# Kernel tuning notes

Hardware: AMD Instinct MI355X
Metric: run time of the kernel (lower is better)

The kernel has to match this reference:

```python
import jax, jax.numpy as jnp
import numpy as np
import math

B, S, D = 2, 4096, 512
H = 8
DH = D // H  # 64


def setup_inputs() -> dict:
    key = jax.random.key(0)
    k1, k2, k3, k4, k5 = jax.random.split(key, 5)
    scale = 1.0 / math.sqrt(D)
    return {
        "x": jax.random.normal(k1, (B, S, D), dtype=jnp.float32),
        "W_in": jax.random.normal(k2, (D, 3 * D), dtype=jnp.float32) * scale,
        "b_in": jax.random.normal(k3, (3 * D,), dtype=jnp.float32) * 0.01,
        "W_out": jax.random.normal(k4, (D, D), dtype=jnp.float32) * scale,
        "b_out": jax.random.normal(k5, (D,), dtype=jnp.float32) * 0.01,
        "causal_mask": 1,
    }


def reference(x, W_in, b_in, W_out, b_out, causal_mask):
    b, s, d = x.shape
    # fused QKV projection: (b, s, 3d)
    qkv = x @ W_in + b_in
    q, k, v = jnp.split(qkv, 3, axis=-1)
    # (b, s, d) -> (b, h, s, dh)
    def to_heads(t):
        return t.reshape(b, s, H, DH).transpose(0, 2, 1, 3)
    q, k, v = to_heads(q), to_heads(k), to_heads(v)
    # raw scores (b, h, s, s)
    scores = jnp.einsum("bhqd,bhkd->bhqk", q, k)
    if causal_mask:  # static python flag
        # upper-triangular (strictly above diag) -> -inf, applied pre-scaling
        # (matches source; -inf invariant under /sqrt(d_head))
        tri = jnp.triu(jnp.ones((s, s), dtype=bool), k=1)
        scores = jnp.where(tri, -jnp.inf, scores)
    attn = jax.nn.softmax(scores / math.sqrt(DH), axis=-1)
    out = jnp.einsum("bhqk,bhkd->bhqd", attn, v)
    out = out.transpose(0, 2, 1, 3).reshape(b, s, d)
    return out @ W_out + b_out
```

## Files before the change

### kernel.cpp

```cpp
#include <hip/hip_runtime.h>
#include <cstdint>
#include <cmath>

typedef unsigned short BF16;
typedef __attribute__((ext_vector_type(8))) short short8;
typedef __attribute__((ext_vector_type(4))) float f32x4;
typedef __attribute__((ext_vector_type(16))) float f32x16;
typedef __attribute__((ext_vector_type(2))) unsigned int uint2v;
typedef __attribute__((ext_vector_type(4))) unsigned int uint4v;

#define S_LEN 4096
#define DMODEL 512
#define NHEAD 8
#define DHEAD 64
#define BS 2
#define NROWS (BS * NHEAD * S_LEN)

__device__ __forceinline__ BF16 f2bf(float f) {
  union { float f; uint32_t u; } v; v.f = f;
  uint32_t r = (v.u + 0x7FFFu + ((v.u >> 16) & 1u)) >> 16;
  return (BF16)r;
}

__device__ __forceinline__ float bf2f(short u) {
  return __uint_as_float(((unsigned)(unsigned short)u) << 16);
}

__device__ __forceinline__ unsigned cvtpk(float a, float b) {
  unsigned r;
  asm volatile("v_cvt_pk_bf16_f32 %0, %1, %2" : "=v"(r) : "v"(a), "v"(b));
  return r;
}

__device__ __forceinline__ float partner32(float x, int hi) {
  unsigned a = __float_as_uint(x), b = a;
  uint2v r = __builtin_amdgcn_permlane32_swap(a, b, false, false);
  return __uint_as_float(hi ? r[0] : r[1]);
}

__device__ __forceinline__ void pl32(unsigned &a, unsigned &b) {
  uint2v r = __builtin_amdgcn_permlane32_swap(a, b, false, false);
  a = r[0]; b = r[1];
}

__device__ __forceinline__ void gload16(const void* g, void* lds) {
  __builtin_amdgcn_global_load_lds(
      (const __attribute__((address_space(1))) void*)g,
      (__attribute__((address_space(3))) void*)lds, 16, 0, 0);
}

#define MAX3(a, b, c) fmaxf(fmaxf((a), (b)), (c))
#define CS_CONST 0.18033688011112042f

__global__ __launch_bounds__(256) void cvt_x_k(const float* __restrict__ x,
                                               BF16* __restrict__ xb) {
  int i = blockIdx.x * 256 + threadIdx.x;
  float4 v = reinterpret_cast<const float4*>(x)[i];
  ushort4 o;
  o.x = f2bf(v.x); o.y = f2bf(v.y); o.z = f2bf(v.z); o.w = f2bf(v.w);
  reinterpret_cast<ushort4*>(xb)[i] = o;
}

__global__ __launch_bounds__(256) void trw_k(const float* __restrict__ W_in,
                                             const float* __restrict__ W_out,
                                             BF16* __restrict__ wint,
                                             BF16* __restrict__ woutt) {
  __shared__ float t[32][33];
  const bool second = blockIdx.x >= 48;
  const float* W = second ? W_out : W_in;
  BF16* Wt = second ? woutt : wint;
  const int N = second ? DMODEL : 3 * DMODEL;
  const int K = DMODEL;
  int n0 = (second ? ((int)blockIdx.x - 48) : (int)blockIdx.x) * 32;
  int k0 = blockIdx.y * 32;
  int tx = threadIdx.x & 31, ty = threadIdx.x >> 5;
#pragma unroll
  for (int i = 0; i < 4; ++i)
    t[ty + 8 * i][tx] = W[(size_t)(k0 + ty + 8 * i) * N + n0 + tx];
  __syncthreads();
#pragma unroll
  for (int i = 0; i < 4; ++i)
    Wt[(size_t)(n0 + ty + 8 * i) * K + k0 + tx] = f2bf(t[tx][ty + 8 * i]);
}

template <int MODE>
__global__ __launch_bounds__(256)
void gemm_k(const BF16* __restrict__ A, const BF16* __restrict__ Bt,
            const float* __restrict__ bias,
            BF16* __restrict__ Qb, BF16* __restrict__ Kb, BF16* __restrict__ Vc,
            float* __restrict__ Out) {
  __shared__ BF16 As[128 * 64];
  __shared__ BF16 Bs[128 * 64];
  const int tid = threadIdx.x;
  const int l = tid & 63, w = tid >> 6;
  const int wm = w >> 1, wn = w & 1;
  const int bm = blockIdx.x, bn = blockIdx.y;
  f32x4 acc[4][4] = {};

  for (int kt = 0; kt < 512 / 64; ++kt) {
#pragma unroll
    for (int i = 0; i < 4; ++i) {
      int ldsoff = i * 4096 + w * 1024;
      int off = ldsoff + l * 16;
      int row = off >> 7;
      int slot = ((off >> 4) & 7) ^ (row & 7);
      gload16(A + (size_t)(bm * 128 + row) * 512 + kt * 64 + slot * 8,
              (char*)As + ldsoff);
      gload16(Bt + (size_t)(bn * 128 + row) * 512 + kt * 64 + slot * 8,
              (char*)Bs + ldsoff);
    }
    __syncthreads();
    const char* Ab = (const char*)As;
    const char* Bb = (const char*)Bs;
    short8 af[4][2], bfr[4][2];
#pragma unroll
    for (int mf = 0; mf < 4; ++mf)
#pragma unroll
      for (int kk = 0; kk < 2; ++kk) {
        int row = wm * 64 + mf * 16 + (l & 15);
        int slot = ((l >> 4) + 4 * kk) ^ (row & 7);
        af[mf][kk] = *(const short8*)(Ab + row * 128 + slot * 16);
      }
#pragma unroll
    for (int nf = 0; nf < 4; ++nf)
#pragma unroll
      for (int kk = 0; kk < 2; ++kk) {
        int row = wn * 64 + nf * 16 + (l & 15);
        int slot = ((l >> 4) + 4 * kk) ^ (row & 7);
        bfr[nf][kk] = *(const short8*)(Bb + row * 128 + slot * 16);
      }
    __builtin_amdgcn_s_setprio(1);
#pragma unroll
    for (int kk = 0; kk < 2; ++kk)
#pragma unroll
      for (int mf = 0; mf < 4; ++mf)
#pragma unroll
        for (int nf = 0; nf < 4; ++nf)
          acc[mf][nf] = __builtin_amdgcn_mfma_f32_16x16x32_bf16(
              af[mf][kk], bfr[nf][kk], acc[mf][nf], 0, 0, 0);
    __builtin_amdgcn_s_setprio(0);
    __syncthreads();
  }

#pragma unroll
  for (int mf = 0; mf < 4; ++mf)
#pragma unroll
    for (int nf = 0; nf < 4; ++nf)
#pragma unroll
      for (int r = 0; r < 4; ++r) {
        int row = bm * 128 + wm * 64 + mf * 16 + ((l >> 4) << 2) + r;
        int col = bn * 128 + wn * 64 + nf * 16 + (l & 15);
        float v = acc[mf][nf][r] + bias[col];
        if (MODE == 0) {
          int sec = col >> 9, nl = col & 511;
          int h = nl >> 6, dh = nl & 63;
          int b = row >> 12, s = row & 4095;
          BF16* dst = sec == 0 ? Qb : (sec == 1 ? Kb : Vc);
          dst[(((size_t)(b * NHEAD + h)) * S_LEN + s) * DHEAD + dh] = f2bf(v);
        } else {
          Out[(size_t)row * DMODEL + col] = v;
        }
      }
}

__global__ __launch_bounds__(256)
void v_tr_k(const BF16* __restrict__ Vc, BF16* __restrict__ Vt) {
  __shared__ BF16 t[64][66];
  const int bh = blockIdx.y, st = blockIdx.x;
  const int tid = threadIdx.x;
  const int g = tid >> 3, c8 = (tid & 7) * 8;
#pragma unroll
  for (int p = 0; p < 2; ++p) {
    int s = p * 32 + g;
    short8 v = *(const short8*)(Vc + ((size_t)bh * S_LEN + st * 64 + s) * DHEAD + c8);
#pragma unroll
    for (int j = 0; j < 8; ++j) t[s][c8 + j] = (BF16)(unsigned short)v[j];
  }
  __syncthreads();
#pragma unroll
  for (int p = 0; p < 2; ++p) {
    int dh = p * 32 + g;
    short8 o;
#pragma unroll
    for (int j = 0; j < 8; ++j) o[j] = (short)t[c8 + j][dh];
    *(short8*)(Vt + ((size_t)bh * DHEAD + dh) * S_LEN + st * 64 + c8) = o;
  }
}

__global__ __launch_bounds__(256, 4)
void attn_k(const BF16* __restrict__ Qg, const BF16* __restrict__ Kg,
            const BF16* __restrict__ Vg, BF16* __restrict__ Opb,
            float* __restrict__ Ml) {
  __shared__ BF16 Kl[2][64 * 64];
  __shared__ BF16 Vl[2][64 * 64];
  const int tid = threadIdx.x, l = tid & 63, w = tid >> 6;
  const int hi = l >> 5, ln = l & 31;
  const int wgid = blockIdx.x;
  const int xcd = wgid & 7, j = wgid >> 3;
  const int bh = xcd * 2 + (j & 1);
  const int qr = (j >> 1) & 3;
  const int p = j >> 3;
  const BF16* Qh = Qg + (size_t)bh * S_LEN * DHEAD;
  const BF16* Kh = Kg + (size_t)bh * S_LEN * DHEAD;
  const BF16* Vh = Vg + (size_t)bh * DHEAD * S_LEN;
  const float CS = CS_CONST;
  short8 ones;
#pragma unroll
  for (int i = 0; i < 8; ++i) ones[i] = (short)0x3F80;

  int cur = 0;
  for (int rep = 0; rep < 2; ++rep) {
    const int qt = rep ? (31 - p) : p;
    const int qq = rep ? (3 - qr) : qr;
    const int NTf = 2 * qt + 2;
    const int kbase = (qq * NTf) >> 2;
    const int kend = ((qq + 1) * NTf) >> 2;
    const int NT = kend - kbase;
    const int q0w = qt * 128 + w * 32;
    const int qrow = q0w + ln;
    __syncthreads();

    short8 qb[4];
    {
      const BF16* qp = Qh + (size_t)qrow * DHEAD + hi * 8;
#pragma unroll
      for (int ks = 0; ks < 4; ++ks) qb[ks] = *(const short8*)(qp + ks * 16);
    }
    f32x16 oacc0 = {}, oacc1 = {}, lacc = {};
    float m_ = -INFINITY;

    auto stage = [&](int buf, int ktile) {
      const int kv0 = ktile * 64;
#pragma unroll
      for (int i = 0; i < 2; ++i) {
        int base = i * 4096 + w * 1024;
        int off = base + l * 16;
        int row = off >> 7;
        int slot = ((off >> 4) & 7) ^ (row & 7);
        gload16(Kh + (size_t)(kv0 + row) * DHEAD + slot * 8, (char*)Kl[buf] + base);
        gload16(Vh + (size_t)row * S_LEN + kv0 + slot * 8, (char*)Vl[buf] + base);
      }
    };

    if (NT > 0) {
      stage(cur, kbase);
      for (int kt = 0; kt < NT; ++kt) {
        __syncthreads();
        if (kt + 1 < NT) stage(cur ^ 1, kbase + kt + 1);
        const int kv0 = (kbase + kt) * 64;
        if (kv0 <= q0w + 31) {
          const char* Kb_ = (const char*)Kl[cur];
          f32x16 s0 = {}, s1 = {};
          __builtin_amdgcn_s_setprio(1);
#pragma unroll
          for (int ks = 0; ks < 4; ++ks) {
            int slot0 = (2 * ks + hi) ^ (ln & 7);
            short8 kf0 = *(const short8*)(Kb_ + ln * 128 + slot0 * 16);
            int row1 = 32 + ln;
            int slot1 = (2 * ks + hi) ^ (row1 & 7);
            short8 kf1 = *(const short8*)(Kb_ + row1 * 128 + slot1 * 16);
            s0 = __builtin_amdgcn_mfma_f32_32x32x16_bf16(kf0, qb[ks], s0, 0, 0, 0);
            s1 = __builtin_amdgcn_mfma_f32_32x32x16_bf16(kf1, qb[ks], s1, 0, 0, 0);
          }
          __builtin_amdgcn_s_setprio(0);
          if (kv0 + 63 > q0w) {
#pragma unroll
            for (int r = 0; r < 16; ++r) {
              int crow = (r & 3) + 8 * (r >> 2) + 4 * hi;
              if (kv0 + crow > qrow) s0[r] = -INFINITY;
              if (kv0 + 32 + crow > qrow) s1[r] = -INFINITY;
            }
          }
          float a0 = MAX3(s0[0], s0[1], s0[2]);
          float a1 = MAX3(s0[3], s0[4], s0[5]);
          float a2 = MAX3(s0[6], s0[7], s0[8]);
          float a3 = MAX3(s0[9], s0[10], s0[11]);
          float a4 = MAX3(s0[12], s0[13], s0[14]);
          float a5 = MAX3(s0[15], s1[0], s1[1]);
          float a6 = MAX3(s1[2], s1[3], s1[4]);
          float a7 = MAX3(s1[5], s1[6], s1[7]);
          float a8 = MAX3(s1[8], s1[9], s1[10]);
          float a9 = MAX3(s1[11], s1[12], s1[13]);
          float a10 = fmaxf(s1[14], s1[15]);
          float b0 = MAX3(a0, a1, a2);
          float b1 = MAX3(a3, a4, a5);
          float b2 = MAX3(a6, a7, a8);
          float b3 = fmaxf(a9, a10);
          float pmax = fmaxf(fmaxf(b0, b1), fmaxf(b2, b3));
          pmax = fmaxf(pmax, partner32(pmax, hi));
          bool need = (pmax - m_) * CS > 8.0f;
          if (__any(need)) {
            float mn = fmaxf(m_, pmax);
            float alpha = exp2f((m_ - mn) * CS);
            m_ = mn;
            lacc[0] *= alpha;
#pragma unroll
            for (int r = 0; r < 16; ++r) { oacc0[r] *= alpha; oacc1[r] *= alpha; }
          }
          const float mb = m_ * CS;
          float p0[16], p1[16];
#pragma unroll
          for (int r = 0; r < 16; ++r) p0[r] = exp2f(fmaf(s0[r], CS, -mb));
#pragma unroll
          for (int r = 0; r < 16; ++r) p1[r] = exp2f(fmaf(s1[r], CS, -mb));
          short8 pf[4];
#pragma unroll
          for (int hf = 0; hf < 2; ++hf) {
            const float* pp = hf ? p1 : p0;
            unsigned w01 = cvtpk(pp[0], pp[1]), w23 = cvtpk(pp[2], pp[3]);
            unsigned w45 = cvtpk(pp[4], pp[5]), w67 = cvtpk(pp[6], pp[7]);
            unsigned w89 = cvtpk(pp[8], pp[9]), wab = cvtpk(pp[10], pp[11]);
            unsigned wcd = cvtpk(pp[12], pp[13]), wef = cvtpk(pp[14], pp[15]);
            pl32(w01, w45);
            pl32(w23, w67);
            pl32(w89, wcd);
            pl32(wab, wef);
            union { uint4v u; short8 s; } c0, c1;
            c0.u = (uint4v){w01, w23, w45, w67};
            c1.u = (uint4v){w89, wab, wcd, wef};
            pf[hf * 2 + 0] = c0.s;
            pf[hf * 2 + 1] = c1.s;
          }
          const char* Vb_ = (const char*)Vl[cur];
          __builtin_amdgcn_s_setprio(1);
#pragma unroll
          for (int ks = 0; ks < 4; ++ks) {
            int slot0 = (2 * ks + hi) ^ (ln & 7);
            short8 vf0 = *(const short8*)(Vb_ + ln * 128 + slot0 * 16);
            int row1 = 32 + ln;
            int slot1 = (2 * ks + hi) ^ (row1 & 7);
            short8 vf1 = *(const short8*)(Vb_ + row1 * 128 + slot1 * 16);
            oacc0 = __builtin_amdgcn_mfma_f32_32x32x16_bf16(vf0, pf[ks], oacc0, 0, 0, 0);
            oacc1 = __builtin_amdgcn_mfma_f32_32x32x16_bf16(vf1, pf[ks], oacc1, 0, 0, 0);
            lacc = __builtin_amdgcn_mfma_f32_32x32x16_bf16(ones, pf[ks], lacc, 0, 0, 0);
          }
          __builtin_amdgcn_s_setprio(0);
        }
        cur ^= 1;
      }
    }

    BF16* Op = Opb + ((size_t)qq * NROWS + (size_t)bh * S_LEN + qrow) * DHEAD;
#pragma unroll
    for (int blk = 0; blk < 2; ++blk) {
      const f32x16 oa = blk ? oacc1 : oacc0;
#pragma unroll
      for (int g = 0; g < 4; ++g) {
        int dh0 = 8 * g + 4 * hi + 32 * blk;
        unsigned lo = cvtpk(oa[4 * g + 0], oa[4 * g + 1]);
        unsigned h2 = cvtpk(oa[4 * g + 2], oa[4 * g + 3]);
        uint2v st = {lo, h2};
        *(uint2v*)(Op + dh0) = st;
      }
    }
    if (hi == 0) {
      float2 ml = {m_, lacc[0]};
      *(float2*)(Ml + ((size_t)qq * NROWS + (size_t)bh * S_LEN + qrow) * 2) = ml;
    }
  }
}

__global__ __launch_bounds__(256)
void merge_k(const BF16* __restrict__ Opb, const float* __restrict__ Ml,
             BF16* __restrict__ Ob) {
  const int wv = blockIdx.x * 4 + (threadIdx.x >> 6);
  const int lane = threadIdx.x & 63;
  const int r_off = lane >> 3, c8 = (lane & 7) * 8;
#pragma unroll
  for (int it = 0; it < 4; ++it) {
    int row = wv * 32 + it * 8 + r_off;
    float2 ml0 = *(const float2*)(Ml + (size_t)row * 2);
    float2 ml1 = *(const float2*)(Ml + ((size_t)NROWS + row) * 2);
    float2 ml2 = *(const float2*)(Ml + ((size_t)2 * NROWS + row) * 2);
    float2 ml3 = *(const float2*)(Ml + ((size_t)3 * NROWS + row) * 2);
    float m = fmaxf(fmaxf(ml0.x, ml1.x), fmaxf(ml2.x, ml3.x));
    float a0 = exp2f((ml0.x - m) * CS_CONST);
    float a1 = exp2f((ml1.x - m) * CS_CONST);
    float a2 = exp2f((ml2.x - m) * CS_CONST);
    float a3 = exp2f((ml3.x - m) * CS_CONST);
    float linv = 1.0f / (ml0.y * a0 + ml1.y * a1 + ml2.y * a2 + ml3.y * a3);
    a0 *= linv; a1 *= linv; a2 *= linv; a3 *= linv;
    short8 v0 = *(const short8*)(Opb + ((size_t)0 * NROWS + row) * DHEAD + c8);
    short8 v1 = *(const short8*)(Opb + ((size_t)1 * NROWS + row) * DHEAD + c8);
    short8 v2 = *(const short8*)(Opb + ((size_t)2 * NROWS + row) * DHEAD + c8);
    short8 v3 = *(const short8*)(Opb + ((size_t)3 * NROWS + row) * DHEAD + c8);
    float o[8];
#pragma unroll
    for (int jj = 0; jj < 8; ++jj)
      o[jj] = bf2f(v0[jj]) * a0 + bf2f(v1[jj]) * a1 +
              bf2f(v2[jj]) * a2 + bf2f(v3[jj]) * a3;
    uint4v pk = {cvtpk(o[0], o[1]), cvtpk(o[2], o[3]),
                 cvtpk(o[4], o[5]), cvtpk(o[6], o[7])};
    int bh = row >> 12, s = row & 4095;
    *(uint4v*)(Ob + ((size_t)((bh >> 3) * S_LEN + s)) * DMODEL +
               (bh & 7) * DHEAD + c8) = pk;
  }
}

extern "C" void kernel_launch(void* const* d_in, const int* in_sizes, int n_in,
                              void* d_out, int out_size, void* d_ws, size_t ws_size,
                              hipStream_t stream) {
  const float* x = (const float*)d_in[0];
  const float* W_in = (const float*)d_in[1];
  const float* b_in = (const float*)d_in[2];
  const float* W_out = (const float*)d_in[3];
  const float* b_out = (const float*)d_in[4];
  float* out = (float*)d_out;

  char* ws = (char*)d_ws;
  const size_t SZ_X = (size_t)BS * S_LEN * DMODEL * 2;
  const size_t SZ_OP = (size_t)NROWS * DHEAD * 2;
  BF16* xb    = (BF16*)(ws);
  BF16* Vt    = xb;
  BF16* wint  = (BF16*)(ws + SZ_X);
  BF16* woutt = (BF16*)(ws + SZ_X + 3 * DMODEL * DMODEL * 2);
  BF16* Qb    = (BF16*)(ws + SZ_X + 4 * DMODEL * DMODEL * 2);
  BF16* Kb    = (BF16*)((char*)Qb + SZ_X);
  BF16* Vc    = (BF16*)((char*)Kb + SZ_X);
  BF16* Ob    = (BF16*)((char*)Vc + SZ_X);
  BF16* Opb   = (BF16*)((char*)Ob + SZ_X);
  float* Ml   = (float*)((char*)Opb + 4 * SZ_OP);

  cvt_x_k<<<dim3((BS * S_LEN * DMODEL) / 4 / 256), 256, 0, stream>>>(x, xb);
  trw_k<<<dim3(64, DMODEL / 32), 256, 0, stream>>>(W_in, W_out, wint, woutt);
  gemm_k<0><<<dim3(BS * S_LEN / 128, 3 * DMODEL / 128), 256, 0, stream>>>(
      xb, wint, b_in, Qb, Kb, Vc, nullptr);
  v_tr_k<<<dim3(S_LEN / 64, BS * NHEAD), 256, 0, stream>>>(Vc, Vt);
  attn_k<<<dim3(1024), 256, 0, stream>>>(Qb, Kb, Vt, Opb, Ml);
  merge_k<<<dim3(512), 256, 0, stream>>>(Opb, Ml, Ob);
  gemm_k<1><<<dim3(BS * S_LEN / 128, DMODEL / 128), 256, 0, stream>>>(
      Ob, woutt, b_out, nullptr, nullptr, nullptr, out);
}
```

Baseline: 201.6 us.

## Fuse split-KV merge into output projection GEMM and compute row sums on VALU

The separate merge kernel is removed. The output GEMM now combines the four partial attention outputs with their max/sum statistics while loading its A tiles into shared memory, which eliminates the intermediate Ob buffer round trip and one launch. The cost is that each output-column block redoes the merge, so partial outputs are read several times, and the A loads become synchronous. Separately, the softmax row sum in attention is accumulated with scalar adds and a lane exchange instead of an extra MFMA against a ones vector.

```diff
diff --git a/kernel.cpp b/kernel.cpp
--- a/kernel.cpp
+++ b/kernel.cpp
@@ -83,12 +83,10 @@
     Wt[(size_t)(n0 + ty + 8 * i) * K + k0 + tx] = f2bf(t[tx][ty + 8 * i]);
 }
 
-template <int MODE>
 __global__ __launch_bounds__(256)
-void gemm_k(const BF16* __restrict__ A, const BF16* __restrict__ Bt,
-            const float* __restrict__ bias,
-            BF16* __restrict__ Qb, BF16* __restrict__ Kb, BF16* __restrict__ Vc,
-            float* __restrict__ Out) {
+void gemm_qkv_k(const BF16* __restrict__ A, const BF16* __restrict__ Bt,
+                const float* __restrict__ bias,
+                BF16* __restrict__ Qb, BF16* __restrict__ Kb, BF16* __restrict__ Vc) {
   __shared__ BF16 As[128 * 64];
   __shared__ BF16 Bs[128 * 64];
   const int tid = threadIdx.x;
@@ -151,15 +149,11 @@
         int row = bm * 128 + wm * 64 + mf * 16 + ((l >> 4) << 2) + r;
         int col = bn * 128 + wn * 64 + nf * 16 + (l & 15);
         float v = acc[mf][nf][r] + bias[col];
-        if (MODE == 0) {
-          int sec = col >> 9, nl = col & 511;
-          int h = nl >> 6, dh = nl & 63;
-          int b = row >> 12, s = row & 4095;
-          BF16* dst = sec == 0 ? Qb : (sec == 1 ? Kb : Vc);
-          dst[(((size_t)(b * NHEAD + h)) * S_LEN + s) * DHEAD + dh] = f2bf(v);
-        } else {
-          Out[(size_t)row * DMODEL + col] = v;
-        }
+        int sec = col >> 9, nl = col & 511;
+        int h = nl >> 6, dh = nl & 63;
+        int b = row >> 12, s = row & 4095;
+        BF16* dst = sec == 0 ? Qb : (sec == 1 ? Kb : Vc);
+        dst[(((size_t)(b * NHEAD + h)) * S_LEN + s) * DHEAD + dh] = f2bf(v);
       }
 }
 
@@ -204,9 +198,6 @@
   const BF16* Kh = Kg + (size_t)bh * S_LEN * DHEAD;
   const BF16* Vh = Vg + (size_t)bh * DHEAD * S_LEN;
   const float CS = CS_CONST;
-  short8 ones;
-#pragma unroll
-  for (int i = 0; i < 8; ++i) ones[i] = (short)0x3F80;
 
   int cur = 0;
   for (int rep = 0; rep < 2; ++rep) {
@@ -226,8 +217,8 @@
 #pragma unroll
       for (int ks = 0; ks < 4; ++ks) qb[ks] = *(const short8*)(qp + ks * 16);
     }
-    f32x16 oacc0 = {}, oacc1 = {}, lacc = {};
-    float m_ = -INFINITY;
+    f32x16 oacc0 = {}, oacc1 = {};
+    float m_ = -INFINITY, l_ = 0.f;
 
     auto stage = [&](int buf, int ktile) {
       const int kv0 = ktile * 64;
@@ -293,16 +284,19 @@
             float mn = fmaxf(m_, pmax);
             float alpha = exp2f((m_ - mn) * CS);
             m_ = mn;
-            lacc[0] *= alpha;
+            l_ *= alpha;
 #pragma unroll
             for (int r = 0; r < 16; ++r) { oacc0[r] *= alpha; oacc1[r] *= alpha; }
           }
           const float mb = m_ * CS;
           float p0[16], p1[16];
-#pragma unroll
-          for (int r = 0; r < 16; ++r) p0[r] = exp2f(fmaf(s0[r], CS, -mb));
-#pragma unroll
-          for (int r = 0; r < 16; ++r) p1[r] = exp2f(fmaf(s1[r], CS, -mb));
+          float rs = 0.f;
+#pragma unroll
+          for (int r = 0; r < 16; ++r) { p0[r] = exp2f(fmaf(s0[r], CS, -mb)); rs += p0[r]; }
+#pragma unroll
+          for (int r = 0; r < 16; ++r) { p1[r] = exp2f(fmaf(s1[r], CS, -mb)); rs += p1[r]; }
+          rs += partner32(rs, hi);
+          l_ += rs;
           short8 pf[4];
 #pragma unroll
           for (int hf = 0; hf < 2; ++hf) {
@@ -332,7 +326,6 @@
             short8 vf1 = *(const short8*)(Vb_ + row1 * 128 + slot1 * 16);
             oacc0 = __builtin_amdgcn_mfma_f32_32x32x16_bf16(vf0, pf[ks], oacc0, 0, 0, 0);
             oacc1 = __builtin_amdgcn_mfma_f32_32x32x16_bf16(vf1, pf[ks], oacc1, 0, 0, 0);
-            lacc = __builtin_amdgcn_mfma_f32_32x32x16_bf16(ones, pf[ks], lacc, 0, 0, 0);
           }
           __builtin_amdgcn_s_setprio(0);
         }
@@ -354,47 +347,113 @@
       }
     }
     if (hi == 0) {
-      float2 ml = {m_, lacc[0]};
+      float2 ml = {m_, l_};
       *(float2*)(Ml + ((size_t)qq * NROWS + (size_t)bh * S_LEN + qrow) * 2) = ml;
     }
   }
 }
 
 __global__ __launch_bounds__(256)
-void merge_k(const BF16* __restrict__ Opb, const float* __restrict__ Ml,
-             BF16* __restrict__ Ob) {
-  const int wv = blockIdx.x * 4 + (threadIdx.x >> 6);
-  const int lane = threadIdx.x & 63;
-  const int r_off = lane >> 3, c8 = (lane & 7) * 8;
-#pragma unroll
-  for (int it = 0; it < 4; ++it) {
-    int row = wv * 32 + it * 8 + r_off;
-    float2 ml0 = *(const float2*)(Ml + (size_t)row * 2);
-    float2 ml1 = *(const float2*)(Ml + ((size_t)NROWS + row) * 2);
-    float2 ml2 = *(const float2*)(Ml + ((size_t)2 * NROWS + row) * 2);
-    float2 ml3 = *(const float2*)(Ml + ((size_t)3 * NROWS + row) * 2);
-    float m = fmaxf(fmaxf(ml0.x, ml1.x), fmaxf(ml2.x, ml3.x));
-    float a0 = exp2f((ml0.x - m) * CS_CONST);
-    float a1 = exp2f((ml1.x - m) * CS_CONST);
-    float a2 = exp2f((ml2.x - m) * CS_CONST);
-    float a3 = exp2f((ml3.x - m) * CS_CONST);
-    float linv = 1.0f / (ml0.y * a0 + ml1.y * a1 + ml2.y * a2 + ml3.y * a3);
-    a0 *= linv; a1 *= linv; a2 *= linv; a3 *= linv;
-    short8 v0 = *(const short8*)(Opb + ((size_t)0 * NROWS + row) * DHEAD + c8);
-    short8 v1 = *(const short8*)(Opb + ((size_t)1 * NROWS + row) * DHEAD + c8);
-    short8 v2 = *(const short8*)(Opb + ((size_t)2 * NROWS + row) * DHEAD + c8);
-    short8 v3 = *(const short8*)(Opb + ((size_t)3 * NROWS + row) * DHEAD + c8);
-    float o[8];
-#pragma unroll
-    for (int jj = 0; jj < 8; ++jj)
-      o[jj] = bf2f(v0[jj]) * a0 + bf2f(v1[jj]) * a1 +
-              bf2f(v2[jj]) * a2 + bf2f(v3[jj]) * a3;
-    uint4v pk = {cvtpk(o[0], o[1]), cvtpk(o[2], o[3]),
-                 cvtpk(o[4], o[5]), cvtpk(o[6], o[7])};
-    int bh = row >> 12, s = row & 4095;
-    *(uint4v*)(Ob + ((size_t)((bh >> 3) * S_LEN + s)) * DMODEL +
-               (bh & 7) * DHEAD + c8) = pk;
+void gemm_out_k(const BF16* __restrict__ Opb, const float* __restrict__ Ml,
+                const BF16* __restrict__ Bt, const float* __restrict__ bias,
+                float* __restrict__ Out) {
+  __shared__ BF16 As[128 * 64];
+  __shared__ BF16 Bs[128 * 64];
+  const int tid = threadIdx.x;
+  const int l = tid & 63, w = tid >> 6;
+  const int wm = w >> 1, wn = w & 1;
+  const int bm = blockIdx.x, bn = blockIdx.y;
+  const size_t SL = (size_t)NROWS * DHEAD;
+  f32x4 acc[4][4] = {};
+
+  for (int kt = 0; kt < 512 / 64; ++kt) {
+#pragma unroll
+    for (int i = 0; i < 4; ++i) {
+      int ldsoff = i * 4096 + w * 1024;
+      int off = ldsoff + l * 16;
+      int row = off >> 7;
+      int slot = ((off >> 4) & 7) ^ (row & 7);
+      gload16(Bt + (size_t)(bn * 128 + row) * 512 + kt * 64 + slot * 8,
+              (char*)Bs + ldsoff);
+    }
+#pragma unroll
+    for (int i = 0; i < 4; ++i) {
+      int off = i * 4096 + w * 1024 + l * 16;
+      int row = off >> 7;
+      int dh0 = (off & 127) >> 1;
+      int slot16 = ((off >> 4) & 7) ^ (row & 7);
+      int g = bm * 128 + row;
+      int b = g >> 12, s = g & 4095;
+      size_t mlb = ((size_t)(b * NHEAD + kt)) * S_LEN + s;
+      size_t base = mlb * DHEAD + dh0;
+      short8 v0 = *(const short8*)(Opb + base);
+      short8 v1 = *(const short8*)(Opb + SL + base);
+      short8 v2 = *(const short8*)(Opb + 2 * SL + base);
+      short8 v3 = *(const short8*)(Opb + 3 * SL + base);
+      float2 ml0 = *(const float2*)(Ml + mlb * 2);
+      float2 ml1 = *(const float2*)(Ml + ((size_t)NROWS + mlb) * 2);
+      float2 ml2 = *(const float2*)(Ml + ((size_t)2 * NROWS + mlb) * 2);
+      float2 ml3 = *(const float2*)(Ml + ((size_t)3 * NROWS + mlb) * 2);
+      float m = fmaxf(fmaxf(ml0.x, ml1.x), fmaxf(ml2.x, ml3.x));
+      float a0 = exp2f((ml0.x - m) * CS_CONST);
+      float a1 = exp2f((ml1.x - m) * CS_CONST);
+      float a2 = exp2f((ml2.x - m) * CS_CONST);
+      float a3 = exp2f((ml3.x - m) * CS_CONST);
+      float linv = 1.0f / (ml0.y * a0 + ml1.y * a1 + ml2.y * a2 + ml3.y * a3);
+      a0 *= linv; a1 *= linv; a2 *= linv; a3 *= linv;
+      float o[8];
+#pragma unroll
+      for (int jj = 0; jj < 8; ++jj)
+        o[jj] = bf2f(v0[jj]) * a0 + bf2f(v1[jj]) * a1 +
+                bf2f(v2[jj]) * a2 + bf2f(v3[jj]) * a3;
+      union { uint4v u; short8 s; } pk;
+      pk.u = (uint4v){cvtpk(o[0], o[1]), cvtpk(o[2], o[3]),
+                      cvtpk(o[4], o[5]), cvtpk(o[6], o[7])};
+      *(short8*)((char*)As + row * 128 + slot16 * 16) = pk.s;
+    }
+    __syncthreads();
+    const char* Ab = (const char*)As;
+    const char* Bb = (const char*)Bs;
+    short8 af[4][2], bfr[4][2];
+#pragma unroll
+    for (int mf = 0; mf < 4; ++mf)
+#pragma unroll
+      for (int kk = 0; kk < 2; ++kk) {
+        int row = wm * 64 + mf * 16 + (l & 15);
+        int slot = ((l >> 4) + 4 * kk) ^ (row & 7);
+        af[mf][kk] = *(const short8*)(Ab + row * 128 + slot * 16);
+      }
+#pragma unroll
+    for (int nf = 0; nf < 4; ++nf)
+#pragma unroll
+      for (int kk = 0; kk < 2; ++kk) {
+        int row = wn * 64 + nf * 16 + (l & 15);
+        int slot = ((l >> 4) + 4 * kk) ^ (row & 7);
+        bfr[nf][kk] = *(const short8*)(Bb + row * 128 + slot * 16);
+      }
+    __builtin_amdgcn_s_setprio(1);
+#pragma unroll
+    for (int kk = 0; kk < 2; ++kk)
+#pragma unroll
+      for (int mf = 0; mf < 4; ++mf)
+#pragma unroll
+        for (int nf = 0; nf < 4; ++nf)
+          acc[mf][nf] = __builtin_amdgcn_mfma_f32_16x16x32_bf16(
+              af[mf][kk], bfr[nf][kk], acc[mf][nf], 0, 0, 0);
+    __builtin_amdgcn_s_setprio(0);
+    __syncthreads();
   }
+
+#pragma unroll
+  for (int mf = 0; mf < 4; ++mf)
+#pragma unroll
+    for (int nf = 0; nf < 4; ++nf)
+#pragma unroll
+      for (int r = 0; r < 4; ++r) {
+        int row = bm * 128 + wm * 64 + mf * 16 + ((l >> 4) << 2) + r;
+        int col = bn * 128 + wn * 64 + nf * 16 + (l & 15);
+        Out[(size_t)row * DMODEL + col] = acc[mf][nf][r] + bias[col];
+      }
 }
 
 extern "C" void kernel_launch(void* const* d_in, const int* in_sizes, int n_in,
@@ -417,17 +476,15 @@
   BF16* Qb    = (BF16*)(ws + SZ_X + 4 * DMODEL * DMODEL * 2);
   BF16* Kb    = (BF16*)((char*)Qb + SZ_X);
   BF16* Vc    = (BF16*)((char*)Kb + SZ_X);
-  BF16* Ob    = (BF16*)((char*)Vc + SZ_X);
-  BF16* Opb   = (BF16*)((char*)Ob + SZ_X);
+  BF16* Opb   = (BF16*)((char*)Vc + SZ_X);
   float* Ml   = (float*)((char*)Opb + 4 * SZ_OP);
 
   cvt_x_k<<<dim3((BS * S_LEN * DMODEL) / 4 / 256), 256, 0, stream>>>(x, xb);
   trw_k<<<dim3(64, DMODEL / 32), 256, 0, stream>>>(W_in, W_out, wint, woutt);
-  gemm_k<0><<<dim3(BS * S_LEN / 128, 3 * DMODEL / 128), 256, 0, stream>>>(
-      xb, wint, b_in, Qb, Kb, Vc, nullptr);
+  gemm_qkv_k<<<dim3(BS * S_LEN / 128, 3 * DMODEL / 128), 256, 0, stream>>>(
+      xb, wint, b_in, Qb, Kb, Vc);
   v_tr_k<<<dim3(S_LEN / 64, BS * NHEAD), 256, 0, stream>>>(Vc, Vt);
   attn_k<<<dim3(1024), 256, 0, stream>>>(Qb, Kb, Vt, Opb, Ml);
-  merge_k<<<dim3(512), 256, 0, stream>>>(Opb, Ml, Ob);
-  gemm_k<1><<<dim3(BS * S_LEN / 128, DMODEL / 128), 256, 0, stream>>>(
-      Ob, woutt, b_out, nullptr, nullptr, nullptr, out);
-}
+  gemm_out_k<<<dim3(BS * S_LEN / 128, DMODEL / 128), 256, 0, stream>>>(
+      Opb, Ml, woutt, b_out, out);
+}
```

After: 211.5 us. 4.9% more time.
